# Kernel tuning notes

Measured on AMD Instinct MI355X. Metric: run time of the kernel, lower is better.

## Reference

```python
import jax, jax.numpy as jnp
import numpy as np

B, Nq, C = 1, 40000, 256
Hh, L, P = 8, 4, 8
hd = C // Hh
LEVEL_SHAPES = [(128, 128), (64, 64), (32, 32), (16, 16)]


def setup_inputs() -> dict:
    key = jax.random.key(0)
    ks = jax.random.split(key, 16)
    inp = {}
    inp['query'] = jax.random.normal(ks[0], (B, Nq, C), jnp.float32)
    # reference points in [-1, 1] normalized coords (x, y)
    inp['reference_points'] = jax.random.uniform(ks[1], (B, Nq, L, 2), jnp.float32) * 2.0 - 1.0
    for i, (h, w) in enumerate(LEVEL_SHAPES):
        inp[f'feat{i}'] = jax.random.normal(ks[2 + i], (B, C, h, w), jnp.float32)
    # learned params (torch Linear y = x @ W + b, W stored as [in, out])
    inp['W_off'] = jax.random.normal(ks[6], (C, Hh * L * P * 2), jnp.float32) * 0.02
    inp['b_off'] = jax.random.normal(ks[7], (Hh * L * P * 2,), jnp.float32) * 0.5
    inp['W_attn'] = jax.random.normal(ks[8], (C, Hh * L * P), jnp.float32) * 0.02
    inp['b_attn'] = jnp.zeros((Hh * L * P,), jnp.float32)
    inp['W_val'] = jax.random.normal(ks[9], (C, C), jnp.float32) * (1.0 / np.sqrt(C))
    inp['b_val'] = jnp.zeros((C,), jnp.float32)
    inp['W_out'] = jax.random.normal(ks[10], (C, C), jnp.float32) * (1.0 / np.sqrt(C))
    inp['b_out'] = jnp.zeros((C,), jnp.float32)
    return inp


def _deform_sample(v, coords):
    # Bilinear grid_sample, align_corners=True, zeros padding.
    # v: [B, Hh, H, W, hd]; coords: [B, Hh, S, 2] in [-1, 1] (x, y)
    _, _, H, W, _ = v.shape
    x = (coords[..., 0] + 1.0) * 0.5 * (W - 1)
    y = (coords[..., 1] + 1.0) * 0.5 * (H - 1)
    x0 = jnp.floor(x)
    y0 = jnp.floor(y)
    vflat = v.reshape(v.shape[0], v.shape[1], H * W, v.shape[4])

    def corner(xi, yi, w):
        inb = (xi >= 0) & (xi <= W - 1) & (yi >= 0) & (yi <= H - 1)
        idx = (jnp.clip(yi, 0, H - 1) * W + jnp.clip(xi, 0, W - 1)).astype(jnp.int32)
        g = jnp.take_along_axis(vflat, idx[..., None], axis=2)  # [B,Hh,S,hd]
        return g * (w * inb)[..., None]

    return (corner(x0, y0, (x0 + 1 - x) * (y0 + 1 - y))
            + corner(x0 + 1, y0, (x - x0) * (y0 + 1 - y))
            + corner(x0, y0 + 1, (x0 + 1 - x) * (y - y0))
            + corner(x0 + 1, y0 + 1, (x - x0) * (y - y0)))


def reference(query, feat0, feat1, feat2, feat3, reference_points,
              W_off, b_off, W_attn, b_attn, W_val, b_val, W_out, b_out):
    feats = [feat0, feat1, feat2, feat3]
    off = (query @ W_off + b_off).reshape(B, Nq, Hh, L, P, 2)
    w = (query @ W_attn + b_attn).reshape(B, Nq, Hh, L, P)
    w = jax.nn.softmax(w, axis=-1)  # softmax over points, per level
    # samp: [B, Nq, Hh, L, P, 2]
    samp = reference_points[:, :, None, :, None, :] + jnp.tanh(off) * 0.25

    out = jnp.zeros((B, Nq, Hh, hd), jnp.float32)
    for l, f in enumerate(feats):
        Hl, Wl = f.shape[2], f.shape[3]
        v = jnp.einsum('bchw,cd->bhwd', f, W_val) + b_val  # value proj
        v = v.reshape(B, Hl, Wl, Hh, hd).transpose(0, 3, 1, 2, 4)  # [B,Hh,H,W,hd]
        coords = samp[:, :, :, l].transpose(0, 2, 1, 3, 4).reshape(B, Hh, Nq * P, 2)
        s = _deform_sample(v, coords).reshape(B, Hh, Nq, P, hd)
        wl = w[:, :, :, l].transpose(0, 2, 1, 3)  # [B,Hh,Nq,P]
        out = out + jnp.einsum('bhnpd,bhnp->bnhd', s, wl)

    return out.reshape(B, Nq, C) @ W_out + b_out
```

## Files before the change

### kernel.cpp

```cpp
#include <hip/hip_runtime.h>
#include <hip/hip_fp16.h>
#include <math.h>

#define NQ 40000

typedef short s16x8 __attribute__((ext_vector_type(8)));
typedef float f32x4 __attribute__((ext_vector_type(4)));

static constexpr int HLa[4] = {128, 64, 32, 16};
static constexpr int HWa[4] = {16384, 4096, 1024, 256};
static constexpr int VB[4] = {0, 4194304, 5242880, 5505024};

__device__ __forceinline__ short bf16hi(float x) {
    union { float f; unsigned u; } v; v.f = x;
    unsigned r = v.u + 0x7FFFu + ((v.u >> 16) & 1u);
    return (short)(r >> 16);
}
__device__ __forceinline__ float bf16f(short s) {
    union { unsigned u; float f; } v; v.u = ((unsigned)(unsigned short)s) << 16;
    return v.f;
}
__device__ __forceinline__ float fast_tanh(float x) {
    float xc = fminf(fmaxf(x, -15.f), 15.f);
    float e = __expf(2.f * xc);
    return (e - 1.f) / (e + 1.f);
}
#define MFMA16(a, b, c) __builtin_amdgcn_mfma_f32_16x16x32_bf16(a, b, c, 0, 0, 0)

__global__ __launch_bounds__(256) void prep_w(
    const float* __restrict__ Woff, const float* __restrict__ Wattn,
    const float* __restrict__ Wout, short* __restrict__ WtH, short* __restrict__ WtL)
{
    int r = blockIdx.x, c = threadIdx.x;
    float x;
    if (r < 512)      x = Woff[c * 512 + r];
    else if (r < 768) x = Wattn[c * 256 + (r - 512)];
    else              x = Wout[c * 256 + (r - 768)];
    short hi = bf16hi(x);
    WtH[r * 256 + c] = hi;
    WtL[r * 256 + c] = bf16hi(x - bf16f(hi));
}

__global__ __launch_bounds__(256) void vproj_kernel(
    const float* __restrict__ f0, const float* __restrict__ f1,
    const float* __restrict__ f2, const float* __restrict__ f3,
    const float* __restrict__ Wv, const float* __restrict__ bv,
    __half* __restrict__ v)
{
    __shared__ float fT[256 * 16];

    int bid = blockIdx.x;
    const float* f;
    int base, HWl, hw0;
    if (bid < 1024)      { f = f0; base = VB[0]; HWl = 16384; hw0 = bid * 16; }
    else if (bid < 1280) { f = f1; base = VB[1]; HWl = 4096;  hw0 = (bid - 1024) * 16; }
    else if (bid < 1344) { f = f2; base = VB[2]; HWl = 1024;  hw0 = (bid - 1280) * 16; }
    else                 { f = f3; base = VB[3]; HWl = 256;   hw0 = (bid - 1344) * 16; }

    int t = threadIdx.x;
    for (int k = 0; k < 16; ++k) {
        int idx = k * 256 + t;
        int c = idx >> 4, j = idx & 15;
        fT[idx] = f[c * HWl + hw0 + j];
    }
    __syncthreads();

    int to4 = (t & 63) * 4;
    int hw4 = (t >> 6) * 4;

    float4 bv4 = *(const float4*)(bv + to4);
    float acc[4][4];
    #pragma unroll
    for (int i = 0; i < 4; ++i) {
        acc[i][0] = bv4.x; acc[i][1] = bv4.y; acc[i][2] = bv4.z; acc[i][3] = bv4.w;
    }

    #pragma unroll 4
    for (int c = 0; c < 256; ++c) {
        float4 w4 = *(const float4*)(Wv + c * 256 + to4);
        float4 fv = *(const float4*)(fT + c * 16 + hw4);
        float fa[4] = {fv.x, fv.y, fv.z, fv.w};
        float wa[4] = {w4.x, w4.y, w4.z, w4.w};
        #pragma unroll
        for (int i = 0; i < 4; ++i)
            #pragma unroll
            for (int j = 0; j < 4; ++j)
                acc[i][j] += fa[i] * wa[j];
    }

    int hh = to4 >> 5, dd4 = to4 & 31;
    #pragma unroll
    for (int i = 0; i < 4; ++i) {
        int hw = hw0 + hw4 + i;
        __half2 h0 = __floats2half2_rn(acc[i][0], acc[i][1]);
        __half2 h1 = __floats2half2_rn(acc[i][2], acc[i][3]);
        uint2 st = make_uint2(*(unsigned*)&h0, *(unsigned*)&h1);
        *(uint2*)(v + base + (hh * HWl + hw) * 32 + dd4) = st;
    }
}

__global__ __launch_bounds__(256, 5) void msda_kernel(
    const float* __restrict__ query, const float* __restrict__ refp,
    const float* __restrict__ boff,  const float* __restrict__ battn,
    const float* __restrict__ bout,
    const short* __restrict__ WtH,   const short* __restrict__ WtL,
    const __half* __restrict__ v,    float* __restrict__ out)
{
    __shared__ __align__(16) char lds[29952];
    short*    sQh  = (short*)lds;
    short*    sQl  = (short*)(lds + 8448);
    float*    offL = (float*)lds;
    uint2*    sPWh = (uint2*)(lds + 8448);
    __half*   sWh  = (__half*)(lds + 16896);
    unsigned* sPI  = (unsigned*)(lds + 25344);
    float*    sR   = (float*)(lds + 29440);

    const int t = threadIdx.x;
    const int n0 = blockIdx.x * 16;
    const int wv = t >> 6, lane = t & 63;
    const int mrow = lane & 15, kg = lane >> 4;

    for (int k2 = 0; k2 < 16; ++k2) {
        float x = query[(n0 + k2) * 256 + t];
        short hi = bf16hi(x);
        sQh[k2 * 264 + t] = hi;
        sQl[k2 * 264 + t] = bf16hi(x - bf16f(hi));
    }
    if (t < 128) sR[t] = refp[n0 * 8 + t];
    __syncthreads();

    f32x4 accO[8], accA[4];
    {
        f32x4 z = {0.f, 0.f, 0.f, 0.f};
        #pragma unroll
        for (int j = 0; j < 8; ++j) accO[j] = z;
        #pragma unroll
        for (int j = 0; j < 4; ++j) accA[j] = z;
    }
    {
        const short* offH = WtH + (wv * 128 + mrow) * 256 + kg * 8;
        const short* offLo = WtL + (wv * 128 + mrow) * 256 + kg * 8;
        const short* attH = WtH + (512 + wv * 64 + mrow) * 256 + kg * 8;
        const short* attL = WtL + (512 + wv * 64 + mrow) * 256 + kg * 8;
        const int aoff = mrow * 264 + kg * 8;
        #pragma unroll
        for (int kk = 0; kk < 8; ++kk) {
            s16x8 ah = *(const s16x8*)(sQh + aoff + kk * 32);
            s16x8 al = *(const s16x8*)(sQl + aoff + kk * 32);
            #pragma unroll
            for (int j = 0; j < 8; ++j) {
                s16x8 bh = *(const s16x8*)(offH + j * 4096 + kk * 32);
                s16x8 bl = *(const s16x8*)(offLo + j * 4096 + kk * 32);
                accO[j] = MFMA16(ah, bh, accO[j]);
                accO[j] = MFMA16(al, bh, accO[j]);
                accO[j] = MFMA16(ah, bl, accO[j]);
            }
            #pragma unroll
            for (int ja = 0; ja < 4; ++ja) {
                s16x8 bh = *(const s16x8*)(attH + ja * 4096 + kk * 32);
                s16x8 bl = *(const s16x8*)(attL + ja * 4096 + kk * 32);
                accA[ja] = MFMA16(ah, bh, accA[ja]);
                accA[ja] = MFMA16(al, bh, accA[ja]);
                accA[ja] = MFMA16(ah, bl, accA[ja]);
            }
        }
    }
    #pragma unroll
    for (int j = 0; j < 8; ++j) {
        float bb = boff[wv * 128 + j * 16 + mrow];
        #pragma unroll
        for (int r = 0; r < 4; ++r) accO[j][r] += bb;
    }
    #pragma unroll
    for (int ja = 0; ja < 4; ++ja) {
        float bb = battn[wv * 64 + ja * 16 + mrow];
        #pragma unroll
        for (int r = 0; r < 4; ++r) accA[ja][r] += bb;
    }

    #pragma unroll
    for (int ja = 0; ja < 4; ++ja) {
        int hh = 2 * wv + (ja >> 1);
        int l  = ((ja & 1) << 1) | (mrow >> 3);
        int p  = mrow & 7;
        #pragma unroll
        for (int r = 0; r < 4; ++r) {
            float x = accA[ja][r];
            float m = fmaxf(x, __shfl_xor(x, 1));
            m = fmaxf(m, __shfl_xor(m, 2));
            m = fmaxf(m, __shfl_xor(m, 4));
            float e = __expf(x - m);
            float s = e + __shfl_xor(e, 1);
            s += __shfl_xor(s, 2);
            s += __shfl_xor(s, 4);
            int q = kg * 4 + r;
            sWh[q * 264 + hh * 32 + l * 8 + p] = __float2half_rn(e / s);
        }
    }
    __syncthreads();

    const int clS  = t & 7;
    const int hhLS = (t >> 3) & 1;
    const int qS   = t >> 4;

    for (int k = 0; k < 4; ++k) {
        if (wv == k) {
            #pragma unroll
            for (int j = 0; j < 8; ++j)
                #pragma unroll
                for (int r = 0; r < 4; ++r)
                    offL[(kg * 4 + r) * 132 + j * 16 + mrow] = accO[j][r];
        }
        __syncthreads();

        #pragma unroll
        for (int it = 0; it < 4; ++it) {
            int s = it * 256 + t;
            int q = s >> 6, hhL = (s >> 5) & 1, l = (s >> 3) & 3, p = s & 7;
            const int Wl = 128 >> l;
            const float scl = 0.5f * (float)(Wl - 1);
            float lx = offL[q * 132 + hhL * 64 + l * 16 + p * 2];
            float ly = offL[q * 132 + hhL * 64 + l * 16 + p * 2 + 1];
            float w  = __half2float(sWh[q * 264 + (2 * k + hhL) * 32 + l * 8 + p]);
            float rx = sR[q * 8 + l * 2], ry = sR[q * 8 + l * 2 + 1];
            float cx = rx + fast_tanh(lx) * 0.25f;
            float cy = ry + fast_tanh(ly) * 0.25f;
            float xx = (cx + 1.f) * scl, yy = (cy + 1.f) * scl;
            float x0f = floorf(xx), y0f = floorf(yy);
            float fx = xx - x0f, fy = yy - y0f;
            int x0 = (int)x0f, y0 = (int)y0f;
            int xc0 = min(max(x0, 0), Wl - 1);
            int xc1 = min(max(x0 + 1, 0), Wl - 1);
            int yc0 = min(max(y0, 0), Wl - 1);
            int yc1 = min(max(y0 + 1, 0), Wl - 1);
            bool bx0 = (x0 >= 0) & (x0 < Wl);
            bool bx1 = (x0 + 1 >= 0) & (x0 + 1 < Wl);
            bool by0 = (y0 >= 0) & (y0 < Wl);
            bool by1 = (y0 + 1 >= 0) & (y0 + 1 < Wl);
            float w00 = (bx0 && by0) ? (1.f - fx) * (1.f - fy) * w : 0.f;
            float w01 = (bx1 && by0) ? fx * (1.f - fy) * w : 0.f;
            float w10 = (bx0 && by1) ? (1.f - fx) * fy * w : 0.f;
            float w11 = (bx1 && by1) ? fx * fy * w : 0.f;
            unsigned pw = (unsigned)(yc0 * Wl + xc0)
                        | ((unsigned)(xc1 - xc0) << 14)
                        | ((unsigned)(yc1 - yc0) << 15);
            sPI[s] = pw;
            __half2 hA = __floats2half2_rn(w00, w01);
            __half2 hB = __floats2half2_rn(w10, w11);
            sPWh[s] = make_uint2(*(unsigned*)&hA, *(unsigned*)&hB);
        }
        __syncthreads();

        {
            const int hh = 2 * k + hhLS;
            float ac0 = 0.f, ac1 = 0.f, ac2 = 0.f, ac3 = 0.f;
            #pragma unroll
            for (int l = 0; l < 4; ++l) {
                const int Wl = HLa[l];
                const __half2* vl = (const __half2*)(v + VB[l] + hh * HWa[l] * 32 + clS * 4);
                const int sbase = qS * 64 + hhLS * 32 + l * 8;
                #pragma unroll
                for (int p = 0; p < 8; ++p) {
                    unsigned pw = sPI[sbase + p];
                    uint2 ww = sPWh[sbase + p];
                    int idx = pw & 0x3FFF;
                    int dxo = ((pw >> 14) & 1) * 16;
                    int dyo = ((pw >> 15) & 1) * (Wl * 16);
                    const __half2* b00 = vl + idx * 16;
                    uint2 g00 = *(const uint2*)(b00);
                    uint2 g01 = *(const uint2*)(b00 + dxo);
                    uint2 g10 = *(const uint2*)(b00 + dyo);
                    uint2 g11 = *(const uint2*)(b00 + dxo + dyo);
                    __half2 wA = *(__half2*)&ww.x;
                    __half2 wB = *(__half2*)&ww.y;
                    __half2 w00 = __low2half2(wA),  w01 = __high2half2(wA);
                    __half2 w10 = __low2half2(wB),  w11 = __high2half2(wB);
                    __half2 s0 = __hmul2(w00, *(__half2*)&g00.x);
                    s0 = __hfma2(w01, *(__half2*)&g01.x, s0);
                    s0 = __hfma2(w10, *(__half2*)&g10.x, s0);
                    s0 = __hfma2(w11, *(__half2*)&g11.x, s0);
                    __half2 s1 = __hmul2(w00, *(__half2*)&g00.y);
                    s1 = __hfma2(w01, *(__half2*)&g01.y, s1);
                    s1 = __hfma2(w10, *(__half2*)&g10.y, s1);
                    s1 = __hfma2(w11, *(__half2*)&g11.y, s1);
                    float2 f0 = __half22float2(s0);
                    float2 f1 = __half22float2(s1);
                    ac0 += f0.x; ac1 += f0.y; ac2 += f1.x; ac3 += f1.y;
                }
            }
            __half2 o0 = __floats2half2_rn(ac0, ac1);
            __half2 o1 = __floats2half2_rn(ac2, ac3);
            *(uint2*)(sWh + qS * 264 + hh * 32 + clS * 4) =
                make_uint2(*(unsigned*)&o0, *(unsigned*)&o1);
        }
        __syncthreads();
    }

    {
        int q = t & 15, seg = t >> 4;
        const __half2* src = (const __half2*)(sWh + q * 264 + seg * 16);
        short* dh = sQh + q * 264 + seg * 16;
        short* dl = sQl + q * 264 + seg * 16;
        #pragma unroll
        for (int jj = 0; jj < 8; ++jj) {
            float2 f = __half22float2(src[jj]);
            short h0 = bf16hi(f.x), h1 = bf16hi(f.y);
            dh[2 * jj]     = h0;
            dh[2 * jj + 1] = h1;
            dl[2 * jj]     = bf16hi(f.x - bf16f(h0));
            dl[2 * jj + 1] = bf16hi(f.y - bf16f(h1));
        }
    }
    __syncthreads();

    {
        f32x4 accE[4];
        f32x4 z = {0.f, 0.f, 0.f, 0.f};
        #pragma unroll
        for (int e = 0; e < 4; ++e) accE[e] = z;
        const short* outH = WtH + (768 + wv * 64 + mrow) * 256 + kg * 8;
        const short* outL = WtL + (768 + wv * 64 + mrow) * 256 + kg * 8;
        const int aoff = mrow * 264 + kg * 8;
        #pragma unroll
        for (int kk = 0; kk < 8; ++kk) {
            s16x8 ah = *(const s16x8*)(sQh + aoff + kk * 32);
            s16x8 al = *(const s16x8*)(sQl + aoff + kk * 32);
            #pragma unroll
            for (int e = 0; e < 4; ++e) {
                s16x8 bh = *(const s16x8*)(outH + e * 4096 + kk * 32);
                s16x8 bl = *(const s16x8*)(outL + e * 4096 + kk * 32);
                accE[e] = MFMA16(ah, bh, accE[e]);
                accE[e] = MFMA16(al, bh, accE[e]);
                accE[e] = MFMA16(ah, bl, accE[e]);
            }
        }
        #pragma unroll
        for (int e = 0; e < 4; ++e) {
            int col = wv * 64 + e * 16 + mrow;
            float bb = bout[col];
            #pragma unroll
            for (int r = 0; r < 4; ++r)
                out[(n0 + kg * 4 + r) * 256 + col] = accE[e][r] + bb;
        }
    }
}

extern "C" void kernel_launch(void* const* d_in, const int* in_sizes, int n_in,
                              void* d_out, int out_size, void* d_ws, size_t ws_size,
                              hipStream_t stream) {
    const float* query = (const float*)d_in[0];
    const float* refp  = (const float*)d_in[1];
    const float* f0    = (const float*)d_in[2];
    const float* f1    = (const float*)d_in[3];
    const float* f2    = (const float*)d_in[4];
    const float* f3    = (const float*)d_in[5];
    const float* Woff  = (const float*)d_in[6];
    const float* boff  = (const float*)d_in[7];
    const float* Wattn = (const float*)d_in[8];
    const float* battn = (const float*)d_in[9];
    const float* Wval  = (const float*)d_in[10];
    const float* bval  = (const float*)d_in[11];
    const float* Wout  = (const float*)d_in[12];
    const float* bout  = (const float*)d_in[13];

    __half* v  = (__half*)d_ws;
    short* WtH = (short*)((char*)d_ws + 11141120);
    short* WtL = WtH + 262144;
    float* outp = (float*)d_out;

    prep_w<<<1024, 256, 0, stream>>>(Woff, Wattn, Wout, WtH, WtL);
    vproj_kernel<<<1360, 256, 0, stream>>>(f0, f1, f2, f3, Wval, bval, v);
    msda_kernel<<<2500, 256, 0, stream>>>(query, refp, boff, battn, bout,
                                          WtH, WtL, v, outp);
}
```

Baseline: 563.0 us.

## Swizzle sampling LDS buffers, keep weights in fp32, stage output via LDS

XOR-swizzles the per-sample index and weight arrays in shared memory so that gather-phase reads avoid bank conflicts. Stores attention weights and sampled accumulators in fp32 rather than half, which removes rounding on the intermediate. Stages the final projected output through LDS so that global writes are coalesced float4 rows. The larger LDS footprint forces occupancy down to 4 blocks per CU, which may cost latency hiding in the memory-bound gather.

```diff
diff --git a/kernel.cpp b/kernel.cpp
--- a/kernel.cpp
+++ b/kernel.cpp
@@ -25,6 +25,8 @@
     float e = __expf(2.f * xc);
     return (e - 1.f) / (e + 1.f);
 }
+__device__ __forceinline__ int swzPI(int s) { return s ^ (((s >> 6) & 3) << 3); }
+__device__ __forceinline__ int swzPW(int s) { return s ^ (((s >> 6) & 3) << 2); }
 #define MFMA16(a, b, c) __builtin_amdgcn_mfma_f32_16x16x32_bf16(a, b, c, 0, 0, 0)
 
 __global__ __launch_bounds__(256) void prep_w(
@@ -99,21 +101,21 @@
     }
 }
 
-__global__ __launch_bounds__(256, 5) void msda_kernel(
+__global__ __launch_bounds__(256, 4) void msda_kernel(
     const float* __restrict__ query, const float* __restrict__ refp,
     const float* __restrict__ boff,  const float* __restrict__ battn,
     const float* __restrict__ bout,
     const short* __restrict__ WtH,   const short* __restrict__ WtL,
     const __half* __restrict__ v,    float* __restrict__ out)
 {
-    __shared__ __align__(16) char lds[29952];
+    __shared__ __align__(16) char lds[38144];
     short*    sQh  = (short*)lds;
     short*    sQl  = (short*)(lds + 8448);
     float*    offL = (float*)lds;
     uint2*    sPWh = (uint2*)(lds + 8448);
-    __half*   sWh  = (__half*)(lds + 16896);
-    unsigned* sPI  = (unsigned*)(lds + 25344);
-    float*    sR   = (float*)(lds + 29440);
+    float*    sWf  = (float*)(lds + 16896);
+    unsigned* sPI  = (unsigned*)(lds + 33536);
+    float*    sR   = (float*)(lds + 37632);
 
     const int t = threadIdx.x;
     const int n0 = blockIdx.x * 16;
@@ -194,7 +196,7 @@
             s += __shfl_xor(s, 2);
             s += __shfl_xor(s, 4);
             int q = kg * 4 + r;
-            sWh[q * 264 + hh * 32 + l * 8 + p] = __float2half_rn(e / s);
+            sWf[q * 260 + hh * 32 + l * 8 + p] = e / s;
         }
     }
     __syncthreads();
@@ -221,7 +223,7 @@
             const float scl = 0.5f * (float)(Wl - 1);
             float lx = offL[q * 132 + hhL * 64 + l * 16 + p * 2];
             float ly = offL[q * 132 + hhL * 64 + l * 16 + p * 2 + 1];
-            float w  = __half2float(sWh[q * 264 + (2 * k + hhL) * 32 + l * 8 + p]);
+            float w  = sWf[q * 260 + (2 * k + hhL) * 32 + l * 8 + p];
             float rx = sR[q * 8 + l * 2], ry = sR[q * 8 + l * 2 + 1];
             float cx = rx + fast_tanh(lx) * 0.25f;
             float cy = ry + fast_tanh(ly) * 0.25f;
@@ -244,10 +246,10 @@
             unsigned pw = (unsigned)(yc0 * Wl + xc0)
                         | ((unsigned)(xc1 - xc0) << 14)
                         | ((unsigned)(yc1 - yc0) << 15);
-            sPI[s] = pw;
+            sPI[swzPI(s)] = pw;
             __half2 hA = __floats2half2_rn(w00, w01);
             __half2 hB = __floats2half2_rn(w10, w11);
-            sPWh[s] = make_uint2(*(unsigned*)&hA, *(unsigned*)&hB);
+            sPWh[swzPW(s)] = make_uint2(*(unsigned*)&hA, *(unsigned*)&hB);
         }
         __syncthreads();
 
@@ -261,8 +263,8 @@
                 const int sbase = qS * 64 + hhLS * 32 + l * 8;
                 #pragma unroll
                 for (int p = 0; p < 8; ++p) {
-                    unsigned pw = sPI[sbase + p];
-                    uint2 ww = sPWh[sbase + p];
+                    unsigned pw = sPI[swzPI(sbase + p)];
+                    uint2 ww = sPWh[swzPW(sbase + p)];
                     int idx = pw & 0x3FFF;
                     int dxo = ((pw >> 14) & 1) * 16;
                     int dyo = ((pw >> 15) & 1) * (Wl * 16);
@@ -288,22 +290,20 @@
                     ac0 += f0.x; ac1 += f0.y; ac2 += f1.x; ac3 += f1.y;
                 }
             }
-            __half2 o0 = __floats2half2_rn(ac0, ac1);
-            __half2 o1 = __floats2half2_rn(ac2, ac3);
-            *(uint2*)(sWh + qS * 264 + hh * 32 + clS * 4) =
-                make_uint2(*(unsigned*)&o0, *(unsigned*)&o1);
+            *(float4*)(sWf + qS * 260 + hh * 32 + clS * 4) =
+                make_float4(ac0, ac1, ac2, ac3);
         }
         __syncthreads();
     }
 
     {
         int q = t & 15, seg = t >> 4;
-        const __half2* src = (const __half2*)(sWh + q * 264 + seg * 16);
+        const float* src = sWf + q * 260 + seg * 16;
         short* dh = sQh + q * 264 + seg * 16;
         short* dl = sQl + q * 264 + seg * 16;
         #pragma unroll
         for (int jj = 0; jj < 8; ++jj) {
-            float2 f = __half22float2(src[jj]);
+            float2 f = *(const float2*)(src + 2 * jj);
             short h0 = bf16hi(f.x), h1 = bf16hi(f.y);
             dh[2 * jj]     = h0;
             dh[2 * jj + 1] = h1;
@@ -340,7 +340,16 @@
             float bb = bout[col];
             #pragma unroll
             for (int r = 0; r < 4; ++r)
-                out[(n0 + kg * 4 + r) * 256 + col] = accE[e][r] + bb;
+                sWf[(kg * 4 + r) * 260 + col] = accE[e][r] + bb;
+        }
+    }
+    __syncthreads();
+    {
+        int q = t >> 4, c0 = (t & 15) * 4;
+        #pragma unroll
+        for (int cb = 0; cb < 4; ++cb) {
+            float4 vv = *(const float4*)(sWf + q * 260 + cb * 64 + c0);
+            *(float4*)(out + (n0 + q) * 256 + cb * 64 + c0) = vv;
         }
     }
 }
```

Result: slower. 647.8 us (+15.1%).
